# Optimization experiments

Hardware: AMD Instinct MI355X
Metric: run time of the kernel (lower is better)

Reference implementation:

```python
import jax, jax.numpy as jnp
import numpy as np

N = 100000   # nodes
E = 1250000  # edges per graph
D = 64       # in_feats
H = 64       # hidden_dim
C = 129      # num_classes
EPS = 1e-5


def setup_inputs() -> dict:
    key = jax.random.key(0)
    ks = jax.random.split(key, 32)
    nrm = lambda k, s: jax.random.normal(k, s, jnp.float32) * 0.05
    inp = {
        'node_features': jax.random.normal(ks[0], (N, D), jnp.float32),
        'm_src': jax.random.randint(ks[1], (E,), 0, N, jnp.int32),
        'm_dst': jax.random.randint(ks[2], (E,), 0, N, jnp.int32),
        'r_src': jax.random.randint(ks[3], (E,), 0, N, jnp.int32),
        'r_dst': jax.random.randint(ks[4], (E,), 0, N, jnp.int32),
    }
    i = 5
    for pre in ('soc', 'rt'):
        inp[pre + '_W1'] = nrm(ks[i], (D, H)); inp[pre + '_b1'] = jnp.zeros((H,), jnp.float32)
        inp[pre + '_g1'] = jnp.ones((H,), jnp.float32); inp[pre + '_bt1'] = jnp.zeros((H,), jnp.float32)
        inp[pre + '_W2'] = nrm(ks[i + 1], (H, H)); inp[pre + '_b2'] = jnp.zeros((H,), jnp.float32)
        inp[pre + '_g2'] = jnp.ones((H,), jnp.float32); inp[pre + '_bt2'] = jnp.zeros((H,), jnp.float32)
        i += 2
    inp['gW1'] = nrm(ks[i], (4 * H, H)); inp['gb1'] = jnp.zeros((H,), jnp.float32)
    inp['prelu_a'] = jnp.full((1,), 0.25, jnp.float32)
    inp['gW2'] = nrm(ks[i + 1], (H, H)); inp['gb2'] = jnp.zeros((H,), jnp.float32)
    inp['fcW'] = nrm(ks[i + 2], (H, C)); inp['fcb'] = jnp.zeros((C,), jnp.float32)
    return inp


def _gconv(h, src, dst, W, b):
    # DGL GraphConv, norm='both': D_out^{-1/2} (scatter-sum) D_in^{-1/2}, linear, ELU
    ones = jnp.ones(src.shape[0], jnp.float32)
    deg_o = jax.ops.segment_sum(ones, src, num_segments=N)
    deg_i = jax.ops.segment_sum(ones, dst, num_segments=N)
    ns = jax.lax.rsqrt(jnp.clip(deg_o, 1.0))
    nd = jax.lax.rsqrt(jnp.clip(deg_i, 1.0))
    agg = jax.ops.segment_sum((h * ns[:, None])[src], dst, num_segments=N)
    return jax.nn.elu((agg * nd[:, None]) @ W + b)


def _bn(x, g, b):
    mu = x.mean(0)
    v = x.var(0)
    return (x - mu) * jax.lax.rsqrt(v + EPS) * g + b


def _branch(x, src, dst, W1, b1, g1, bt1, W2, b2, g2, bt2):
    h = _bn(_gconv(x, src, dst, W1, b1), g1, bt1)
    return _bn(_gconv(h, src, dst, W2, b2), g2, bt2)


def reference(node_features, m_src, m_dst, r_src, r_dst,
              soc_W1, soc_b1, soc_g1, soc_bt1, soc_W2, soc_b2, soc_g2, soc_bt2,
              rt_W1, rt_b1, rt_g1, rt_bt1, rt_W2, rt_b2, rt_g2, rt_bt2,
              gW1, gb1, prelu_a, gW2, gb2, fcW, fcb):
    h1 = _branch(node_features, m_src, m_dst, soc_W1, soc_b1, soc_g1, soc_bt1, soc_W2, soc_b2, soc_g2, soc_bt2)
    h2 = _branch(node_features, r_src, r_dst, rt_W1, rt_b1, rt_g1, rt_bt1, rt_W2, rt_b2, rt_g2, rt_bt2)
    cat = jnp.concatenate([h1, h2, jnp.abs(h1 - h2), h1 * h2], axis=-1)
    z = cat @ gW1 + gb1
    z = jnp.where(z > 0, z, prelu_a * z)  # PReLU (single shared slope)
    gate = jax.nn.sigmoid(z @ gW2 + gb2)
    fused = gate * h1 + (1.0 - gate) * h2
    return fused @ fcW + fcb
```

## Files before the change

### kernel.cpp

```cpp
#include <hip/hip_runtime.h>
#include <math.h>

#define NN 100000
#define NE 1250000
#define HD 64
#define NCLS 129
#define NTILES 6250
#define GRID_T 782
#define MAXDEG 64

#define NCH 64
#define CHU ((NE + NCH - 1) / NCH)
#define SUBR 50000
#define NW2 12500
#define NHE2 ((NN + 1) * (size_t)HD)

typedef float f32x4 __attribute__((ext_vector_type(4)));
typedef short bf16x8 __attribute__((ext_vector_type(8)));

__device__ __forceinline__ short f2b(float f) {
    unsigned u = __builtin_bit_cast(unsigned, f);
    u += 0x7FFFu + ((u >> 16) & 1u);
    return (short)(u >> 16);
}
__device__ __forceinline__ float b2f(short s) {
    return __builtin_bit_cast(float, ((unsigned)(unsigned short)s) << 16);
}
__device__ __forceinline__ float uhi(unsigned w) {
    return __builtin_bit_cast(float, w & 0xffff0000u);
}
__device__ __forceinline__ float ulo(unsigned w) {
    return __builtin_bit_cast(float, w << 16);
}

__global__ __launch_bounds__(1024) void k_hist8(
    const int* __restrict__ d0, const int* __restrict__ s0,
    const int* __restrict__ d1, const int* __restrict__ s1,
    unsigned char* __restrict__ P8d, unsigned char* __restrict__ P8s) {
    __shared__ unsigned int hw[NW2];
    int b = blockIdx.x, s = blockIdx.y, z = blockIdx.z;
    int g = z >> 1, arr = z & 1;
    const int* __restrict__ idx = arr ? (g ? s1 : s0) : (g ? d1 : d0);
    for (int i = threadIdx.x; i < NW2; i += 1024) hw[i] = 0;
    __syncthreads();
    int lo = s * SUBR;
    int beg = b * CHU, end = beg + CHU;
    if (end > NE) end = NE;
    for (int i = beg + threadIdx.x; i < end; i += 1024) {
        int v = idx[i] - lo;
        if ((unsigned)v < (unsigned)SUBR)
            atomicAdd(&hw[v >> 2], 1u << ((v & 3) * 8));
    }
    __syncthreads();
    unsigned char* base = arr ? P8s : P8d;
    unsigned int* dst = (unsigned int*)(base + ((size_t)(g * NCH + b)) * NN + lo);
    for (int i = threadIdx.x; i < NW2; i += 1024) dst[i] = hw[i];
}

__global__ void k_reduce8(unsigned int* __restrict__ Pd, const unsigned int* __restrict__ Ps,
                          float* __restrict__ ns, float* __restrict__ nd,
                          int* __restrict__ degi) {
    int w = blockIdx.x * 256 + threadIdx.x;
    if (w >= NN / 4) return;
    int g = blockIdx.y;
    Pd += (size_t)g * NCH * (NN / 4);
    Ps += (size_t)g * NCH * (NN / 4);
    ns += (size_t)g * (NN + 1); nd += (size_t)g * NN; degi += (size_t)g * NN;
    if (w == 0) ns[NN] = 0.f;
    unsigned run = 0;
#pragma unroll 8
    for (int b = 0; b < NCH; ++b) {
        size_t o = (size_t)b * (NN / 4) + w;
        unsigned v = Pd[o];
        Pd[o] = run;
        run += v;
    }
    unsigned so = 0;
#pragma unroll 8
    for (int b = 0; b < NCH; ++b) so += Ps[(size_t)b * (NN / 4) + w];
#pragma unroll
    for (int j = 0; j < 4; ++j) {
        int din = (run >> (8 * j)) & 255;
        int dout = (so >> (8 * j)) & 255;
        int node = w * 4 + j;
        degi[node] = din;
        ns[node] = rsqrtf((float)(dout < 1 ? 1 : dout));
        nd[node] = rsqrtf((float)(din < 1 ? 1 : din));
    }
}

__global__ __launch_bounds__(1024) void k_fill8(
    const int* __restrict__ d0, const int* __restrict__ d1,
    const int* __restrict__ s0, const int* __restrict__ s1,
    const unsigned char* __restrict__ Pofs, int* __restrict__ col) {
    __shared__ unsigned int cur[NW2];
    int b = blockIdx.x, s = blockIdx.y, g = blockIdx.z;
    const int* __restrict__ dst = g ? d1 : d0;
    const int* __restrict__ src = g ? s1 : s0;
    col += ((size_t)g * NN) * MAXDEG;
    const unsigned char* __restrict__ ofs = Pofs + ((size_t)(g * NCH + b)) * NN;
    for (int i = threadIdx.x; i < NW2; i += 1024) cur[i] = 0;
    __syncthreads();
    int lo = s * SUBR;
    int beg = b * CHU, end = beg + CHU;
    if (end > NE) end = NE;
    for (int i = beg + threadIdx.x; i < end; i += 1024) {
        int d = dst[i] - lo;
        if ((unsigned)d < (unsigned)SUBR) {
            unsigned old = atomicAdd(&cur[d >> 2], 1u << ((d & 3) * 8));
            int r = (old >> ((d & 3) * 8)) & 255;
            int node = d + lo;
            col[(size_t)node * MAXDEG + (int)ofs[node] + r] = src[i];
        }
    }
}

__global__ void k_scale_nf(const float* __restrict__ nf, short* __restrict__ T) {
    int i = blockIdx.x * blockDim.x + threadIdx.x;
    if (i >= (NN + 1) * 8) return;
    int node = i >> 3;
    short r[8];
    if (node == NN) {
#pragma unroll
        for (int j = 0; j < 8; ++j) r[j] = 0;
    } else {
        const float4* p = (const float4*)(nf + (size_t)i * 8);
        float4 a = p[0], b = p[1];
        r[0] = f2b(a.x); r[1] = f2b(a.y); r[2] = f2b(a.z); r[3] = f2b(a.w);
        r[4] = f2b(b.x); r[5] = f2b(b.y); r[6] = f2b(b.z); r[7] = f2b(b.w);
    }
    *(bf16x8*)(T + (size_t)i * 8) = *(bf16x8*)r;
}

template <int BN>
__global__ __launch_bounds__(256) void k_gather(
    const short* __restrict__ tab, size_t tabStride,
    const float* __restrict__ ns, const float* __restrict__ nd,
    const int* __restrict__ degi, const int* __restrict__ col,
    short* __restrict__ out, const float* __restrict__ stats,
    const float* __restrict__ ga, const float* __restrict__ gb,
    const float* __restrict__ bta, const float* __restrict__ btb) {
    int w = (blockIdx.x * 256 + threadIdx.x) >> 6;
    int lane = threadIdx.x & 63;
    if (w >= NN) return;
    int g = blockIdx.y;
    tab += (size_t)g * tabStride; nd += (size_t)g * NN; degi += (size_t)g * NN;
    col += ((size_t)g * NN) * MAXDEG; out += (size_t)g * NHE2;
    const float* nsA = ns + (size_t)g * (NN + 1);
    int grp = lane >> 4;
    int sub = lane & 15;
    int deg = degi[w];
    int myc = (lane < deg) ? col[(size_t)w * MAXDEG + lane] : NN;
    float myns = nsA[myc];
    float a0 = 0.f, a1 = 0.f, a2 = 0.f, a3 = 0.f, sl = 0.f;
    for (int j = 0; j < deg; j += 16) {
#pragma unroll
        for (int u = 0; u < 4; ++u) {
            int idx = j + u * 4 + grp;
            int c = __shfl(myc, idx, 64);
            float nsc = __shfl(myns, idx, 64);
            uint2 v = *(const uint2*)(tab + (size_t)c * HD + sub * 4);
            a0 = fmaf(nsc, __builtin_bit_cast(float, v.x << 16), a0);
            a1 = fmaf(nsc, __builtin_bit_cast(float, v.x & 0xffff0000u), a1);
            a2 = fmaf(nsc, __builtin_bit_cast(float, v.y << 16), a2);
            a3 = fmaf(nsc, __builtin_bit_cast(float, v.y & 0xffff0000u), a3);
            if (BN) sl += nsc;
        }
    }
    a0 += __shfl_xor(a0, 16, 64); a1 += __shfl_xor(a1, 16, 64);
    a2 += __shfl_xor(a2, 16, 64); a3 += __shfl_xor(a3, 16, 64);
    a0 += __shfl_xor(a0, 32, 64); a1 += __shfl_xor(a1, 32, 64);
    a2 += __shfl_xor(a2, 32, 64); a3 += __shfl_xor(a3, 32, 64);
    if (BN) { sl += __shfl_xor(sl, 16, 64); sl += __shfl_xor(sl, 32, 64); }
    if (grp == 0) {
        float s = nd[w];
        float r4[4] = {a0, a1, a2, a3};
        if (BN) {
            const float* gp = g ? gb : ga;
            const float* bp = g ? btb : bta;
            const float* st = stats + (size_t)g * 128;
            const float invN = 1.f / (float)NN;
#pragma unroll
            for (int q = 0; q < 4; ++q) {
                int o = sub * 4 + q;
                float mu = st[o] * invN;
                float var = fmaxf(st[64 + o] * invN - mu * mu, 0.f);
                float isd = rsqrtf(var + 1e-5f);
                float sc = gp[o] * isd;
                float sh = bp[o] - mu * sc;
                r4[q] = s * (sc * r4[q] + sh * sl);
            }
        } else {
#pragma unroll
            for (int q = 0; q < 4; ++q) r4[q] *= s;
        }
        unsigned r0 = ((unsigned)(unsigned short)f2b(r4[0])) |
                      (((unsigned)(unsigned short)f2b(r4[1])) << 16);
        unsigned r1 = ((unsigned)(unsigned short)f2b(r4[2])) |
                      (((unsigned)(unsigned short)f2b(r4[3])) << 16);
        uint2 r; r.x = r0; r.y = r1;
        *(uint2*)(out + (size_t)w * HD + sub * 4) = r;
    }
}

__global__ __launch_bounds__(256) void k_lin(
    const short* __restrict__ X, const float* __restrict__ Wa, const float* __restrict__ Wb,
    const float* __restrict__ ba, const float* __restrict__ bb,
    short* __restrict__ Y, float* __restrict__ stats) {
    __shared__ short sW[4096];
    __shared__ float sm2[128];
    int g = blockIdx.y;
    const float* W = g ? Wb : Wa;
    const float* bias = g ? bb : ba;
    X += (size_t)g * NHE2; Y += (size_t)g * NHE2; stats += (size_t)g * 128;
    int t = threadIdx.x;
    for (int i = t; i < 4096; i += 256) {
        int j = i & 7, l16i = (i >> 3) & 15, kgi = (i >> 7) & 3, kbi = (i >> 9) & 1, oti = (i >> 10) & 3;
        sW[i] = f2b(W[(kbi * 32 + kgi * 8 + j) * HD + oti * 16 + l16i]);
    }
    if (t < 128) sm2[t] = 0.f;
    __syncthreads();
    int lane = t & 63, wv = t >> 6, l16 = lane & 15, kg = lane >> 4;
    bf16x8 bfrag[2][4];
#pragma unroll
    for (int kb = 0; kb < 2; ++kb)
#pragma unroll
        for (int ot = 0; ot < 4; ++ot)
            bfrag[kb][ot] = *(const bf16x8*)&sW[((ot * 2 + kb) * 4 + kg) * 128 + l16 * 8];
    float bo[4];
#pragma unroll
    for (int ot = 0; ot < 4; ++ot) bo[ot] = bias[ot * 16 + l16];
    float ps[4] = {0.f, 0.f, 0.f, 0.f}, pq[4] = {0.f, 0.f, 0.f, 0.f};
    for (int tile = blockIdx.x * 4 + wv; tile < NTILES; tile += GRID_T * 4) {
        const short* xp = X + ((size_t)tile * 16 + l16) * HD + kg * 8;
        bf16x8 a0 = *(const bf16x8*)xp;
        bf16x8 a1 = *(const bf16x8*)(xp + 32);
        f32x4 acc[4];
#pragma unroll
        for (int ot = 0; ot < 4; ++ot) {
            acc[ot] = (f32x4){0.f, 0.f, 0.f, 0.f};
            acc[ot] = __builtin_amdgcn_mfma_f32_16x16x32_bf16(a0, bfrag[0][ot], acc[ot], 0, 0, 0);
            acc[ot] = __builtin_amdgcn_mfma_f32_16x16x32_bf16(a1, bfrag[1][ot], acc[ot], 0, 0, 0);
        }
#pragma unroll
        for (int ot = 0; ot < 4; ++ot) {
#pragma unroll
            for (int r = 0; r < 4; ++r) {
                float y = acc[ot][r] + bo[ot];
                y = y > 0.f ? y : expm1f(y);
                ps[ot] += y; pq[ot] += y * y;
                Y[((size_t)tile * 16 + kg * 4 + r) * HD + ot * 16 + l16] = f2b(y);
            }
        }
    }
#pragma unroll
    for (int ot = 0; ot < 4; ++ot) {
        atomicAdd(&sm2[ot * 16 + l16], ps[ot]);
        atomicAdd(&sm2[64 + ot * 16 + l16], pq[ot]);
    }
    __syncthreads();
    if (t < 128) atomicAdd(&stats[t], sm2[t]);
}

#define TRS 72
__global__ __launch_bounds__(256) void k_tail(
    const short* __restrict__ Y1, const short* __restrict__ Y2,
    const float* __restrict__ stats2,
    const float* __restrict__ g2a, const float* __restrict__ g2b,
    const float* __restrict__ bt2a, const float* __restrict__ bt2b,
    const float* __restrict__ W1, const float* __restrict__ bias1,
    const float* __restrict__ pa,
    const float* __restrict__ W2, const float* __restrict__ bias2,
    const float* __restrict__ Wf, const float* __restrict__ biasf,
    float* __restrict__ out) {
    __shared__ short sW1[16384];
    __shared__ short sW2[4096];
    __shared__ short sWf[9216];
    __shared__ short tr[4][2][16 * TRS];
    int t = threadIdx.x;
    for (int i = t; i < 16384; i += 256) {
        int j = i & 7, l16i = (i >> 3) & 15, kgi = (i >> 7) & 3, kbi = (i >> 9) & 7, oti = (i >> 12) & 3;
        sW1[i] = f2b(W1[(kbi * 32 + kgi * 8 + j) * HD + oti * 16 + l16i]);
    }
    for (int i = t; i < 4096; i += 256) {
        int j = i & 7, l16i = (i >> 3) & 15, kgi = (i >> 7) & 3, kbi = (i >> 9) & 1, oti = (i >> 10) & 3;
        sW2[i] = f2b(W2[(kbi * 32 + kgi * 8 + j) * HD + oti * 16 + l16i]);
    }
    for (int i = t; i < 9216; i += 256) {
        int j = i & 7, l16i = (i >> 3) & 15, kgi = (i >> 7) & 3, kbi = (i >> 9) & 1, oti = i >> 10;
        int k = kbi * 32 + kgi * 8 + j, o = oti * 16 + l16i;
        sWf[i] = (o < NCLS) ? f2b(Wf[k * NCLS + o]) : (short)0;
    }
    __syncthreads();
    int lane = t & 63, wv = t >> 6, l16 = lane & 15, kg = lane >> 4;
    float slope = pa[0];
    const float invN = 1.f / (float)NN;
    auto mkc = [&](const float* st, const float* gp, const float* bp, int o) -> unsigned {
        float mu = st[o] * invN;
        float var = fmaxf(st[64 + o] * invN - mu * mu, 0.f);
        float isd = rsqrtf(var + 1e-5f);
        float sc = gp[o] * isd;
        float sh = bp[o] - mu * sc;
        return (((unsigned)(unsigned short)f2b(sc)) << 16) | (unsigned)(unsigned short)f2b(sh);
    };
    unsigned cE0[8], cO0[8], cE1[8], cO1[8];
#pragma unroll
    for (int j = 0; j < 8; ++j) {
        int oe = kg * 8 + j, oo = 32 + kg * 8 + j;
        cE0[j] = mkc(stats2, g2a, bt2a, oe);
        cO0[j] = mkc(stats2, g2a, bt2a, oo);
        cE1[j] = mkc(stats2 + 128, g2b, bt2b, oe);
        cO1[j] = mkc(stats2 + 128, g2b, bt2b, oo);
    }
    float bo1[4], bo2[4], bof[9];
#pragma unroll
    for (int ot = 0; ot < 4; ++ot) { bo1[ot] = bias1[ot * 16 + l16]; bo2[ot] = bias2[ot * 16 + l16]; }
#pragma unroll
    for (int ot = 0; ot < 9; ++ot) {
        int o = ot * 16 + l16;
        bof[ot] = (o < NCLS) ? biasf[o] : 0.f;
    }
    bf16x8 b2frag[2][4];
#pragma unroll
    for (int kb = 0; kb < 2; ++kb)
#pragma unroll
        for (int ot = 0; ot < 4; ++ot)
            b2frag[kb][ot] = *(const bf16x8*)&sW2[((ot * 2 + kb) * 4 + kg) * 128 + l16 * 8];
    short* trZ = &tr[wv][0][0];
    short* trG = &tr[wv][1][0];

    for (int tile = blockIdx.x * 4 + wv; tile < NTILES; tile += GRID_T * 4) {
        size_t rb = ((size_t)tile * 16 + l16) * HD + kg * 8;
        bf16x8 y1e = *(const bf16x8*)(Y1 + rb);
        bf16x8 y1o = *(const bf16x8*)(Y1 + rb + 32);
        bf16x8 y2e = *(const bf16x8*)(Y2 + rb);
        bf16x8 y2o = *(const bf16x8*)(Y2 + rb + 32);
        short b1e[8], b1o[8], b2e[8], b2o[8];
#pragma unroll
        for (int j = 0; j < 8; ++j) {
            b1e[j] = f2b(fmaf(uhi(cE0[j]), b2f(y1e[j]), ulo(cE0[j])));
            b1o[j] = f2b(fmaf(uhi(cO0[j]), b2f(y1o[j]), ulo(cO0[j])));
            b2e[j] = f2b(fmaf(uhi(cE1[j]), b2f(y2e[j]), ulo(cE1[j])));
            b2o[j] = f2b(fmaf(uhi(cO1[j]), b2f(y2o[j]), ulo(cO1[j])));
        }
        bf16x8 h1e = *(bf16x8*)b1e, h1o = *(bf16x8*)b1o;
        bf16x8 h2e = *(bf16x8*)b2e, h2o = *(bf16x8*)b2o;
        bf16x8 fe[8];
        fe[0] = h1e; fe[1] = h1o; fe[2] = h2e; fe[3] = h2o;
        short tabs[8], tprd[8];
#pragma unroll
        for (int j = 0; j < 8; ++j) {
            float a = b2f(h1e[j]), b = b2f(h2e[j]);
            tabs[j] = f2b(fabsf(a - b)); tprd[j] = f2b(a * b);
        }
        fe[4] = *(bf16x8*)tabs; fe[6] = *(bf16x8*)tprd;
#pragma unroll
        for (int j = 0; j < 8; ++j) {
            float a = b2f(h1o[j]), b = b2f(h2o[j]);
            tabs[j] = f2b(fabsf(a - b)); tprd[j] = f2b(a * b);
        }
        fe[5] = *(bf16x8*)tabs; fe[7] = *(bf16x8*)tprd;
        f32x4 acc[4];
#pragma unroll
        for (int ot = 0; ot < 4; ++ot) acc[ot] = (f32x4){0.f, 0.f, 0.f, 0.f};
#pragma unroll
        for (int kb = 0; kb < 8; ++kb)
#pragma unroll
            for (int ot = 0; ot < 4; ++ot) {
                bf16x8 bf = *(const bf16x8*)&sW1[((ot * 8 + kb) * 4 + kg) * 128 + l16 * 8];
                acc[ot] = __builtin_amdgcn_mfma_f32_16x16x32_bf16(fe[kb], bf, acc[ot], 0, 0, 0);
            }
#pragma unroll
        for (int ot = 0; ot < 4; ++ot)
#pragma unroll
            for (int r = 0; r < 4; ++r) {
                float z = acc[ot][r] + bo1[ot];
                z = z > 0.f ? z : slope * z;
                trZ[(kg * 4 + r) * TRS + ot * 16 + l16] = f2b(z);
            }
        asm volatile("s_waitcnt lgkmcnt(0)" ::: "memory");
        __builtin_amdgcn_sched_barrier(0);
        bf16x8 za0 = *(const bf16x8*)&trZ[l16 * TRS + kg * 8];
        bf16x8 za1 = *(const bf16x8*)&trZ[l16 * TRS + 32 + kg * 8];
        f32x4 acc2[4];
#pragma unroll
        for (int ot = 0; ot < 4; ++ot) {
            acc2[ot] = (f32x4){0.f, 0.f, 0.f, 0.f};
            acc2[ot] = __builtin_amdgcn_mfma_f32_16x16x32_bf16(za0, b2frag[0][ot], acc2[ot], 0, 0, 0);
            acc2[ot] = __builtin_amdgcn_mfma_f32_16x16x32_bf16(za1, b2frag[1][ot], acc2[ot], 0, 0, 0);
        }
#pragma unroll
        for (int ot = 0; ot < 4; ++ot)
#pragma unroll
            for (int r = 0; r < 4; ++r) {
                float y = acc2[ot][r] + bo2[ot];
                float gate = 1.f / (1.f + expf(-y));
                trG[(kg * 4 + r) * TRS + ot * 16 + l16] = f2b(gate);
            }
        asm volatile("s_waitcnt lgkmcnt(0)" ::: "memory");
        __builtin_amdgcn_sched_barrier(0);
        bf16x8 ga0 = *(const bf16x8*)&trG[l16 * TRS + kg * 8];
        bf16x8 ga1 = *(const bf16x8*)&trG[l16 * TRS + 32 + kg * 8];
        short f0[8], f1[8];
#pragma unroll
        for (int j = 0; j < 8; ++j) {
            float gf = b2f(ga0[j]);
            f0[j] = f2b(gf * b2f(h1e[j]) + (1.f - gf) * b2f(h2e[j]));
            float gf2 = b2f(ga1[j]);
            f1[j] = f2b(gf2 * b2f(h1o[j]) + (1.f - gf2) * b2f(h2o[j]));
        }
        bf16x8 fa0 = *(bf16x8*)f0, fa1 = *(bf16x8*)f1;
        f32x4 acc3[9];
#pragma unroll
        for (int ot = 0; ot < 9; ++ot) acc3[ot] = (f32x4){0.f, 0.f, 0.f, 0.f};
#pragma unroll
        for (int kb = 0; kb < 2; ++kb) {
            bf16x8 a = kb ? fa1 : fa0;
#pragma unroll
            for (int ot = 0; ot < 9; ++ot) {
                bf16x8 bf = *(const bf16x8*)&sWf[((ot * 2 + kb) * 4 + kg) * 128 + l16 * 8];
                acc3[ot] = __builtin_amdgcn_mfma_f32_16x16x32_bf16(a, bf, acc3[ot], 0, 0, 0);
            }
        }
#pragma unroll
        for (int ot = 0; ot < 9; ++ot) {
            int o = ot * 16 + l16;
            if (o < NCLS) {
#pragma unroll
                for (int r = 0; r < 4; ++r) {
                    int node = tile * 16 + kg * 4 + r;
                    out[(size_t)node * NCLS + o] = acc3[ot][r] + bof[ot];
                }
            }
        }
    }
}

extern "C" void kernel_launch(void* const* d_in, const int* in_sizes, int n_in,
                              void* d_out, int out_size, void* d_ws, size_t ws_size,
                              hipStream_t stream) {
    (void)in_sizes; (void)n_in; (void)out_size; (void)ws_size;
    const int N = NN;

    const float* nf = (const float*)d_in[0];
    const int* m_src = (const int*)d_in[1];
    const int* m_dst = (const int*)d_in[2];
    const int* r_src = (const int*)d_in[3];
    const int* r_dst = (const int*)d_in[4];
    const float *W1[2], *b1[2], *g1[2], *bt1[2], *W2[2], *b2[2], *g2[2], *bt2[2];
    for (int br = 0; br < 2; ++br) {
        int base = 5 + br * 8;
        W1[br] = (const float*)d_in[base + 0];
        b1[br] = (const float*)d_in[base + 1];
        g1[br] = (const float*)d_in[base + 2];
        bt1[br] = (const float*)d_in[base + 3];
        W2[br] = (const float*)d_in[base + 4];
        b2[br] = (const float*)d_in[base + 5];
        g2[br] = (const float*)d_in[base + 6];
        bt2[br] = (const float*)d_in[base + 7];
    }
    const float* gW1 = (const float*)d_in[21];
    const float* gb1 = (const float*)d_in[22];
    const float* pa  = (const float*)d_in[23];
    const float* gW2 = (const float*)d_in[24];
    const float* gb2 = (const float*)d_in[25];
    const float* fcW = (const float*)d_in[26];
    const float* fcb = (const float*)d_in[27];
    float* out = (float*)d_out;

    char* p = (char*)d_ws;
    auto take = [&](size_t bytes) { char* r = p; p += (bytes + 255) & ~(size_t)255; return r; };
    size_t NHb2 = NHE2 * 2;
    unsigned char* P8d = (unsigned char*)take((size_t)2 * NCH * NN);
    unsigned char* P8s = (unsigned char*)take((size_t)2 * NCH * NN);
    int* col  = (int*)take((size_t)2 * NN * MAXDEG * 4);
    short* T  = (short*)take(NHb2);
    short* X  = (short*)take(2 * NHb2);
    short* Y  = (short*)take(2 * NHb2);
    float* ns = (float*)take((size_t)2 * (N + 1) * 4);
    float* nd = (float*)take((size_t)2 * N * 4);
    float* stats = (float*)take(2 * 2 * 128 * 4);
    int* degi = (int*)take((size_t)2 * N * 4);

    int gEWz = ((N + 1) * 8 + 255) / 256;
    int gW4 = (N / 4 + 255) / 256;
    int gGat = (N * 64) / 256;

    k_hist8<<<dim3(NCH, 2, 4), 1024, 0, stream>>>(m_dst, m_src, r_dst, r_src, P8d, P8s);
    k_reduce8<<<dim3(gW4, 2), 256, 0, stream>>>((unsigned int*)P8d, (const unsigned int*)P8s,
                                                ns, nd, degi);
    k_fill8<<<dim3(NCH, 2, 2), 1024, 0, stream>>>(m_dst, r_dst, m_src, r_src, P8d, col);
    hipMemsetAsync(stats, 0, 2 * 2 * 128 * 4, stream);

    k_scale_nf<<<gEWz, 256, 0, stream>>>(nf, T);
    k_gather<0><<<dim3(gGat, 2), 256, 0, stream>>>(T, 0, ns, nd, degi, col, X,
                                                   nullptr, nullptr, nullptr, nullptr, nullptr);
    k_lin<<<dim3(GRID_T, 2), 256, 0, stream>>>(X, W1[0], W1[1], b1[0], b1[1], Y, stats);

    k_gather<1><<<dim3(gGat, 2), 256, 0, stream>>>(Y, NHE2, ns, nd, degi, col, X,
                                                   stats, g1[0], g1[1], bt1[0], bt1[1]);
    k_lin<<<dim3(GRID_T, 2), 256, 0, stream>>>(X, W2[0], W2[1], b2[0], b2[1], Y, stats + 256);

    k_tail<<<GRID_T, 256, 0, stream>>>(Y, Y + NHE2, stats + 256,
                                       g2[0], g2[1], bt2[0], bt2[1],
                                       gW1, gb1, pa, gW2, gb2, fcW, fcb, out);
}
```

Baseline: 368.1 us.

## Fuse neighbor gather with MFMA linear layer into one kernel

Merges the gather (neighbor aggregation with degree/BN scaling) and the bf16 MFMA linear+ELU+stats kernel into a single kernel. Each wave aggregates 16 nodes sequentially into an LDS tile and then runs the MFMA on it. This removes the intermediate X buffer write and read and two kernel launches. In exchange the gather now runs one node per wave iteration inside a grid-stride loop with GRID_T blocks, which lowers parallelism and memory-latency hiding compared with the old one-wave-per-node launch.

```diff
diff --git a/kernel.cpp b/kernel.cpp
--- a/kernel.cpp
+++ b/kernel.cpp
@@ -14,6 +14,7 @@
 #define SUBR 50000
 #define NW2 12500
 #define NHE2 ((NN + 1) * (size_t)HD)
+#define TRS 72
 
 typedef float f32x4 __attribute__((ext_vector_type(4)));
 typedef short bf16x8 __attribute__((ext_vector_type(8)));
@@ -133,86 +134,25 @@
 }
 
 template <int BN>
-__global__ __launch_bounds__(256) void k_gather(
+__global__ __launch_bounds__(256) void k_gl(
     const short* __restrict__ tab, size_t tabStride,
     const float* __restrict__ ns, const float* __restrict__ nd,
     const int* __restrict__ degi, const int* __restrict__ col,
-    short* __restrict__ out, const float* __restrict__ stats,
+    const float* __restrict__ Wa, const float* __restrict__ Wb,
+    const float* __restrict__ ba, const float* __restrict__ bb,
+    short* __restrict__ Y, float* __restrict__ statsOut,
+    const float* __restrict__ statsIn,
     const float* __restrict__ ga, const float* __restrict__ gb,
     const float* __restrict__ bta, const float* __restrict__ btb) {
-    int w = (blockIdx.x * 256 + threadIdx.x) >> 6;
-    int lane = threadIdx.x & 63;
-    if (w >= NN) return;
-    int g = blockIdx.y;
-    tab += (size_t)g * tabStride; nd += (size_t)g * NN; degi += (size_t)g * NN;
-    col += ((size_t)g * NN) * MAXDEG; out += (size_t)g * NHE2;
-    const float* nsA = ns + (size_t)g * (NN + 1);
-    int grp = lane >> 4;
-    int sub = lane & 15;
-    int deg = degi[w];
-    int myc = (lane < deg) ? col[(size_t)w * MAXDEG + lane] : NN;
-    float myns = nsA[myc];
-    float a0 = 0.f, a1 = 0.f, a2 = 0.f, a3 = 0.f, sl = 0.f;
-    for (int j = 0; j < deg; j += 16) {
-#pragma unroll
-        for (int u = 0; u < 4; ++u) {
-            int idx = j + u * 4 + grp;
-            int c = __shfl(myc, idx, 64);
-            float nsc = __shfl(myns, idx, 64);
-            uint2 v = *(const uint2*)(tab + (size_t)c * HD + sub * 4);
-            a0 = fmaf(nsc, __builtin_bit_cast(float, v.x << 16), a0);
-            a1 = fmaf(nsc, __builtin_bit_cast(float, v.x & 0xffff0000u), a1);
-            a2 = fmaf(nsc, __builtin_bit_cast(float, v.y << 16), a2);
-            a3 = fmaf(nsc, __builtin_bit_cast(float, v.y & 0xffff0000u), a3);
-            if (BN) sl += nsc;
-        }
-    }
-    a0 += __shfl_xor(a0, 16, 64); a1 += __shfl_xor(a1, 16, 64);
-    a2 += __shfl_xor(a2, 16, 64); a3 += __shfl_xor(a3, 16, 64);
-    a0 += __shfl_xor(a0, 32, 64); a1 += __shfl_xor(a1, 32, 64);
-    a2 += __shfl_xor(a2, 32, 64); a3 += __shfl_xor(a3, 32, 64);
-    if (BN) { sl += __shfl_xor(sl, 16, 64); sl += __shfl_xor(sl, 32, 64); }
-    if (grp == 0) {
-        float s = nd[w];
-        float r4[4] = {a0, a1, a2, a3};
-        if (BN) {
-            const float* gp = g ? gb : ga;
-            const float* bp = g ? btb : bta;
-            const float* st = stats + (size_t)g * 128;
-            const float invN = 1.f / (float)NN;
-#pragma unroll
-            for (int q = 0; q < 4; ++q) {
-                int o = sub * 4 + q;
-                float mu = st[o] * invN;
-                float var = fmaxf(st[64 + o] * invN - mu * mu, 0.f);
-                float isd = rsqrtf(var + 1e-5f);
-                float sc = gp[o] * isd;
-                float sh = bp[o] - mu * sc;
-                r4[q] = s * (sc * r4[q] + sh * sl);
-            }
-        } else {
-#pragma unroll
-            for (int q = 0; q < 4; ++q) r4[q] *= s;
-        }
-        unsigned r0 = ((unsigned)(unsigned short)f2b(r4[0])) |
-                      (((unsigned)(unsigned short)f2b(r4[1])) << 16);
-        unsigned r1 = ((unsigned)(unsigned short)f2b(r4[2])) |
-                      (((unsigned)(unsigned short)f2b(r4[3])) << 16);
-        uint2 r; r.x = r0; r.y = r1;
-        *(uint2*)(out + (size_t)w * HD + sub * 4) = r;
-    }
-}
-
-__global__ __launch_bounds__(256) void k_lin(
-    const short* __restrict__ X, const float* __restrict__ Wa, const float* __restrict__ Wb,
-    const float* __restrict__ ba, const float* __restrict__ bb,
-    short* __restrict__ Y, float* __restrict__ stats) {
     __shared__ short sW[4096];
     __shared__ float sm2[128];
+    __shared__ short tl[4][16 * TRS];
     int g = blockIdx.y;
     const float* W = g ? Wb : Wa;
     const float* bias = g ? bb : ba;
-    X += (size_t)g * NHE2; Y += (size_t)g * NHE2; stats += (size_t)g * 128;
+    tab += (size_t)g * tabStride; nd += (size_t)g * NN; degi += (size_t)g * NN;
+    col += ((size_t)g * NN) * MAXDEG; Y += (size_t)g * NHE2; statsOut += (size_t)g * 128;
+    const float* nsA = ns + (size_t)g * (NN + 1);
     int t = threadIdx.x;
     for (int i = t; i < 4096; i += 256) {
         int j = i & 7, l16i = (i >> 3) & 15, kgi = (i >> 7) & 3, kbi = (i >> 9) & 1, oti = (i >> 10) & 3;
@@ -221,6 +161,7 @@
     if (t < 128) sm2[t] = 0.f;
     __syncthreads();
     int lane = t & 63, wv = t >> 6, l16 = lane & 15, kg = lane >> 4;
+    int grp = kg, sub = l16;
     bf16x8 bfrag[2][4];
 #pragma unroll
     for (int kb = 0; kb < 2; ++kb)
@@ -230,17 +171,75 @@
     float bo[4];
 #pragma unroll
     for (int ot = 0; ot < 4; ++ot) bo[ot] = bias[ot * 16 + l16];
+    const float* gp = g ? gb : ga;
+    const float* bp = g ? btb : bta;
+    const float* st = BN ? (statsIn + (size_t)g * 128) : nullptr;
+    const float invN = 1.f / (float)NN;
     float ps[4] = {0.f, 0.f, 0.f, 0.f}, pq[4] = {0.f, 0.f, 0.f, 0.f};
+    short* myT = &tl[wv][0];
+
     for (int tile = blockIdx.x * 4 + wv; tile < NTILES; tile += GRID_T * 4) {
-        const short* xp = X + ((size_t)tile * 16 + l16) * HD + kg * 8;
-        bf16x8 a0 = *(const bf16x8*)xp;
-        bf16x8 a1 = *(const bf16x8*)(xp + 32);
+        for (int n = 0; n < 16; ++n) {
+            int w = tile * 16 + n;
+            int deg = degi[w];
+            int myc = (lane < deg) ? col[(size_t)w * MAXDEG + lane] : NN;
+            float myns = nsA[myc];
+            float a0 = 0.f, a1 = 0.f, a2 = 0.f, a3 = 0.f, sl = 0.f;
+            for (int j = 0; j < deg; j += 16) {
+#pragma unroll
+                for (int u = 0; u < 4; ++u) {
+                    int idx = j + u * 4 + grp;
+                    int c = __shfl(myc, idx, 64);
+                    float nsc = __shfl(myns, idx, 64);
+                    uint2 v = *(const uint2*)(tab + (size_t)c * HD + sub * 4);
+                    a0 = fmaf(nsc, ulo(v.x), a0);
+                    a1 = fmaf(nsc, uhi(v.x), a1);
+                    a2 = fmaf(nsc, ulo(v.y), a2);
+                    a3 = fmaf(nsc, uhi(v.y), a3);
+                    if (BN) sl += nsc;
+                }
+            }
+            a0 += __shfl_xor(a0, 16, 64); a1 += __shfl_xor(a1, 16, 64);
+            a2 += __shfl_xor(a2, 16, 64); a3 += __shfl_xor(a3, 16, 64);
+            a0 += __shfl_xor(a0, 32, 64); a1 += __shfl_xor(a1, 32, 64);
+            a2 += __shfl_xor(a2, 32, 64); a3 += __shfl_xor(a3, 32, 64);
+            if (BN) { sl += __shfl_xor(sl, 16, 64); sl += __shfl_xor(sl, 32, 64); }
+            if (grp == 0) {
+                float s = nd[w];
+                float r4[4] = {a0, a1, a2, a3};
+                if (BN) {
+#pragma unroll
+                    for (int q = 0; q < 4; ++q) {
+                        int o = sub * 4 + q;
+                        float mu = st[o] * invN;
+                        float var = fmaxf(st[64 + o] * invN - mu * mu, 0.f);
+                        float isd = rsqrtf(var + 1e-5f);
+                        float sc = gp[o] * isd;
+                        float sh = bp[o] - mu * sc;
+                        r4[q] = s * (sc * r4[q] + sh * sl);
+                    }
+                } else {
+#pragma unroll
+                    for (int q = 0; q < 4; ++q) r4[q] *= s;
+                }
+                unsigned r0 = ((unsigned)(unsigned short)f2b(r4[0])) |
+                              (((unsigned)(unsigned short)f2b(r4[1])) << 16);
+                unsigned r1 = ((unsigned)(unsigned short)f2b(r4[2])) |
+                              (((unsigned)(unsigned short)f2b(r4[3])) << 16);
+                uint2 r; r.x = r0; r.y = r1;
+                *(uint2*)(myT + n * TRS + sub * 4) = r;
+            }
+        }
+        asm volatile("s_waitcnt lgkmcnt(0)" ::: "memory");
+        __builtin_amdgcn_sched_barrier(0);
+        bf16x8 a0f = *(const bf16x8*)&myT[l16 * TRS + kg * 8];
+        bf16x8 a1f = *(const bf16x8*)&myT[l16 * TRS + 32 + kg * 8];
         f32x4 acc[4];
 #pragma unroll
         for (int ot = 0; ot < 4; ++ot) {
             acc[ot] = (f32x4){0.f, 0.f, 0.f, 0.f};
-            acc[ot] = __builtin_amdgcn_mfma_f32_16x16x32_bf16(a0, bfrag[0][ot], acc[ot], 0, 0, 0);
-            acc[ot] = __builtin_amdgcn_mfma_f32_16x16x32_bf16(a1, bfrag[1][ot], acc[ot], 0, 0, 0);
+            acc[ot] = __builtin_amdgcn_mfma_f32_16x16x32_bf16(a0f, bfrag[0][ot], acc[ot], 0, 0, 0);
+            acc[ot] = __builtin_amdgcn_mfma_f32_16x16x32_bf16(a1f, bfrag[1][ot], acc[ot], 0, 0, 0);
         }
 #pragma unroll
         for (int ot = 0; ot < 4; ++ot) {
@@ -259,10 +258,9 @@
         atomicAdd(&sm2[64 + ot * 16 + l16], pq[ot]);
     }
     __syncthreads();
-    if (t < 128) atomicAdd(&stats[t], sm2[t]);
-}
-
-#define TRS 72
+    if (t < 128) atomicAdd(&statsOut[t], sm2[t]);
+}
+
 __global__ __launch_bounds__(256) void k_tail(
     const short* __restrict__ Y1, const short* __restrict__ Y2,
     const float* __restrict__ stats2,
@@ -475,8 +473,8 @@
     unsigned char* P8s = (unsigned char*)take((size_t)2 * NCH * NN);
     int* col  = (int*)take((size_t)2 * NN * MAXDEG * 4);
     short* T  = (short*)take(NHb2);
-    short* X  = (short*)take(2 * NHb2);
-    short* Y  = (short*)take(2 * NHb2);
+    short* Y1 = (short*)take(2 * NHb2);
+    short* Y2 = (short*)take(2 * NHb2);
     float* ns = (float*)take((size_t)2 * (N + 1) * 4);
     float* nd = (float*)take((size_t)2 * N * 4);
     float* stats = (float*)take(2 * 2 * 128 * 4);
@@ -484,7 +482,6 @@
 
     int gEWz = ((N + 1) * 8 + 255) / 256;
     int gW4 = (N / 4 + 255) / 256;
-    int gGat = (N * 64) / 256;
 
     k_hist8<<<dim3(NCH, 2, 4), 1024, 0, stream>>>(m_dst, m_src, r_dst, r_src, P8d, P8s);
     k_reduce8<<<dim3(gW4, 2), 256, 0, stream>>>((unsigned int*)P8d, (const unsigned int*)P8s,
@@ -493,15 +490,15 @@
     hipMemsetAsync(stats, 0, 2 * 2 * 128 * 4, stream);
 
     k_scale_nf<<<gEWz, 256, 0, stream>>>(nf, T);
-    k_gather<0><<<dim3(gGat, 2), 256, 0, stream>>>(T, 0, ns, nd, degi, col, X,
-                                                   nullptr, nullptr, nullptr, nullptr, nullptr);
-    k_lin<<<dim3(GRID_T, 2), 256, 0, stream>>>(X, W1[0], W1[1], b1[0], b1[1], Y, stats);
-
-    k_gather<1><<<dim3(gGat, 2), 256, 0, stream>>>(Y, NHE2, ns, nd, degi, col, X,
-                                                   stats, g1[0], g1[1], bt1[0], bt1[1]);
-    k_lin<<<dim3(GRID_T, 2), 256, 0, stream>>>(X, W2[0], W2[1], b2[0], b2[1], Y, stats + 256);
-
-    k_tail<<<GRID_T, 256, 0, stream>>>(Y, Y + NHE2, stats + 256,
+    k_gl<0><<<dim3(GRID_T, 2), 256, 0, stream>>>(T, 0, ns, nd, degi, col,
+                                                 W1[0], W1[1], b1[0], b1[1], Y1, stats,
+                                                 nullptr, nullptr, nullptr, nullptr, nullptr);
+
+    k_gl<1><<<dim3(GRID_T, 2), 256, 0, stream>>>(Y1, NHE2, ns, nd, degi, col,
+                                                 W2[0], W2[1], b2[0], b2[1], Y2, stats + 256,
+                                                 stats, g1[0], g1[1], bt1[0], bt1[1]);
+
+    k_tail<<<GRID_T, 256, 0, stream>>>(Y2, Y2 + NHE2, stats + 256,
                                        g2[0], g2[1], bt2[0], bt2[1],
                                        gW1, gb1, pa, gW2, gb2, fcW, fcb, out);
 }
```

New measurement: 423.1 us. 14.9% more time.
